# Kernel tuning notes

Hardware: AMD Instinct MI355X
Metric: run time of the kernel (lower is better)

The kernel has to match this reference:

```python
import jax, jax.numpy as jnp
import numpy as np

B = 128          # number of trees
DEPTH = 8        # complete binary tree depth -> 2^8-1 nodes per tree
NPT = 2 ** DEPTH - 1          # 255 nodes per tree
N = B * NPT                   # 32640 total nodes
E_T = NPT - 1                 # 254 edges per tree
F_IN = 64
H = 256


def _build_trees():
    """Complete binary trees; children of local node i are 2i+1, 2i+2."""
    idx = np.arange(NPT)
    depth = np.floor(np.log2(idx + 1)).astype(np.int64)
    order = (DEPTH - 1) - depth                 # leaves=0, root=DEPTH-1
    internal = idx[: NPT // 2]                  # nodes that have children
    parents = np.repeat(internal, 2)
    children = np.empty_like(parents)
    children[0::2] = 2 * internal + 1
    children[1::2] = 2 * internal + 2
    adj_local = np.stack([parents, children], axis=1)        # [E_T, 2]
    offs = (np.arange(B) * NPT)[:, None, None]
    adjacency = (adj_local[None, :, :] + offs).reshape(-1, 2)  # [B*E_T, 2]
    node_order = np.tile(order, B)                             # [N]
    edge_order = np.tile(order[parents], B)                    # [B*E_T]
    return node_order, adjacency, edge_order


def setup_inputs() -> dict:
    key = jax.random.key(0)
    ks = jax.random.split(key, 8)
    node_order, adjacency_list, edge_order = _build_trees()
    s = lambda k, shape, fan: jax.random.normal(k, shape, jnp.float32) * (fan ** -0.5)
    return {
        "features": jax.random.normal(ks[0], (N, F_IN), jnp.float32),
        "node_order": jnp.asarray(node_order, jnp.int32),
        "adjacency_list": jnp.asarray(adjacency_list, jnp.int32),
        "edge_order": jnp.asarray(edge_order, jnp.int32),
        "W_iou_w": s(ks[1], (3 * H, F_IN), F_IN),
        "W_iou_b": jnp.zeros((3 * H,), jnp.float32),
        "U_iou_w": s(ks[2], (3 * H, H), H),
        "W_f_w": s(ks[3], (H, F_IN), F_IN),
        "W_f_b": jnp.zeros((H,), jnp.float32),
        "U_f_w": s(ks[4], (H, H), H),
        "lin0_w": s(ks[5], (H, H), H),
        "lin0_b": jnp.zeros((H,), jnp.float32),
        "lin1_w": s(ks[6], (1, H), H),
        "lin1_b": jnp.zeros((1,), jnp.float32),
    }


def reference(features, node_order, adjacency_list, edge_order,
              W_iou_w, W_iou_b, U_iou_w, W_f_w, W_f_b, U_f_w,
              lin0_w, lin0_b, lin1_w, lin1_b):
    n = features.shape[0]
    parent = adjacency_list[:, 0]
    child = adjacency_list[:, 1]
    # input->gate projections, computed once for all nodes
    wx_iou = features @ W_iou_w.T + W_iou_b      # [N, 3H]
    wx_f = features @ W_f_w.T + W_f_b            # [N, H]
    h = jnp.zeros((n, H), features.dtype)
    c = jnp.zeros((n, H), features.dtype)
    # sequential bottom-up sweep over topological levels (static DEPTH levels)
    for t in range(DEPTH):
        nmask = (node_order == t)[:, None]
        emask = (edge_order == t).astype(features.dtype)[:, None]
        child_h = h[child]                       # [E, H] gather
        h_sum = jax.ops.segment_sum(child_h * emask, parent, num_segments=n)
        iou = wx_iou + h_sum @ U_iou_w.T         # [N, 3H]; h_sum==0 at level 0
        i, o, u = jnp.split(iou, 3, axis=1)
        i = jax.nn.sigmoid(i); o = jax.nn.sigmoid(o); u = jnp.tanh(u)
        f = jax.nn.sigmoid(wx_f[parent] + child_h @ U_f_w.T)  # [E, H]
        c_sum = jax.ops.segment_sum(f * c[child] * emask, parent, num_segments=n)
        new_c = i * u + c_sum
        new_h = o * jnp.tanh(new_c)
        h = jnp.where(nmask, new_h, h)
        c = jnp.where(nmask, new_c, c)
    # unbatch + mean-pool per tree (use_root=False); equal-size trees -> reshape
    x = h.reshape(B, NPT, H).mean(axis=1)        # [B, H]
    # MLP head: Linear -> ReLU -> (dropout inactive in eval) -> Linear
    x = x @ lin0_w.T + lin0_b
    x = jax.nn.relu(x)
    x = x @ lin1_w.T + lin1_b                    # [B, 1]
    return x.reshape(-1)                         # flattened, aux output is None
```

## Files before the change

kernel.cpp:

```cpp
#include <hip/hip_runtime.h>

#define B_TREES 128
#define NPT 255
#define NTOT (B_TREES * NPT)
#define FIN 64
#define HH 256

typedef short bf16x8 __attribute__((ext_vector_type(8)));
typedef float f32x4  __attribute__((ext_vector_type(4)));
typedef unsigned short u16;

__device__ __forceinline__ float sigf(float x) {
    return __frcp_rn(1.0f + __expf(-x));
}
__device__ __forceinline__ float tanh_fast(float x) {
    return __builtin_fmaf(2.0f, sigf(2.0f * x), -1.0f);
}
__device__ __forceinline__ u16 bf_hi(float v) {
    unsigned u = __float_as_uint(v);
    return (u16)((u + 0x7FFFu + ((u >> 16) & 1u)) >> 16);
}
__device__ __forceinline__ float bf_f(u16 b) { return __uint_as_float(((unsigned)b) << 16); }

__global__ __launch_bounds__(256) void pack_B(
    const float* __restrict__ Uiou, const float* __restrict__ Uf,
    const float* __restrict__ Wiou, const float* __restrict__ Wf,
    u16* __restrict__ Bhi, u16* __restrict__ Blo)
{
    int idx = blockIdx.x * 256 + threadIdx.x;
    int j    = idx & 7;
    int lane = (idx >> 3) & 63;
    int ksl  = (idx >> 9) % 10;
    int ct   = idx / 5120;
    int s = ct % 5, hb = ct / 5;
    int n = lane & 15, q = lane >> 4;
    int jH = hb * 16 + n;
    int k = (s < 4 ? ksl * 32 : 320 + ksl * 32) + q * 8 + j;

    float v = 0.0f;
    if (s == 4) {
        if (k < 576) v = Uf[(size_t)jH * HH + (k - 320)];
    } else {
        if (k < 256) {
            v = (s < 3) ? Uiou[(size_t)(s * 256 + jH) * HH + k]
                        : Uf[(size_t)jH * HH + k];
        } else {
            int kw = k - 256;
            v = (s < 3) ? Wiou[(size_t)(s * 256 + jH) * FIN + kw]
                        : 2.0f * Wf[(size_t)jH * FIN + kw];
        }
    }
    u16 hi = bf_hi(v);
    u16 lo = bf_hi(v - bf_f(hi));
    Bhi[idx] = hi;
    Blo[idx] = lo;
}

template<int NCT, bool LEAF>
__global__ __launch_bounds__(256, 2) void level_mfma(
    const float* __restrict__ feat,
    const u16* __restrict__ Bhi, const u16* __restrict__ Blo,
    const float* __restrict__ biou, const float* __restrict__ bfv,
    float* __restrict__ h, float* __restrict__ c,
    int Lt, int lg)
{
    constexpr int CSPLIT = 20 / NCT;
    constexpr int SUBS = NCT / 5;
    __shared__ char smem[73728];
    short* Ahi = (short*)smem;
    short* Alo = (short*)(smem + 36864);

    const int tid = threadIdx.x;
    const int lane = tid & 63, w = tid >> 6;
    const int cs = blockIdx.x % CSPLIT;
    const int rb = blockIdx.x / CSPLIT;
    const int m0 = rb * 32;
    const int msk = (1 << lg) - 1;
    const int ctbase = cs * 4 * NCT + w * NCT;

    const float4* Hf4 = (const float4*)h;
    const float4* Ff4 = (const float4*)feat;

    if constexpr (!LEAF) {
        for (int rep = 0; rep < 8; ++rep) {
            int flat = rep * 256 + tid;
            int m = flat >> 6, f4 = flat & 63;
            int mg = m0 + m;
            int b = mg >> lg, ii = Lt + (mg & msk);
            int gc = b * NPT + 2 * ii + 1;
            float4 h1 = Hf4[(size_t)gc * 64 + f4];
            float4 h2 = Hf4[(size_t)(gc + 1) * 64 + f4];
            float hsv[4] = {h1.x + h2.x, h1.y + h2.y, h1.z + h2.z, h1.w + h2.w};
            float hdv[4] = {h1.x - h2.x, h1.y - h2.y, h1.z - h2.z, h1.w - h2.w};
            int rt = m >> 4, lm = m & 15;
            int ks = f4 >> 3;
            int lane_ = lm + 16 * ((f4 >> 1) & 3);
            int j0 = (f4 & 1) * 4;
            ushort4 sh, sl, dh, dl;
            u16* shp = (u16*)&sh; u16* slp = (u16*)&sl;
            u16* dhp = (u16*)&dh; u16* dlp = (u16*)&dl;
#pragma unroll
            for (int e = 0; e < 4; ++e) {
                u16 a = bf_hi(hsv[e]); shp[e] = a; slp[e] = bf_hi(hsv[e] - bf_f(a));
                u16 d = bf_hi(hdv[e]); dhp[e] = d; dlp[e] = bf_hi(hdv[e] - bf_f(d));
            }
            int base_s = ((rt * 18 + ks) * 64 + lane_) * 8 + j0;
            int base_d = ((rt * 18 + ks + 10) * 64 + lane_) * 8 + j0;
            *(ushort4*)&Ahi[base_s] = sh;  *(ushort4*)&Alo[base_s] = sl;
            *(ushort4*)&Ahi[base_d] = dh;  *(ushort4*)&Alo[base_d] = dl;
        }
    }
    for (int rep = 0; rep < 2; ++rep) {
        int flat = rep * 256 + tid;
        int m = flat >> 4, f4 = flat & 15;
        int mg = m0 + m;
        int b = mg >> lg, ii = Lt + (mg & msk);
        int g = b * NPT + ii;
        float4 x4 = Ff4[(size_t)g * 16 + f4];
        float xv[4] = {x4.x, x4.y, x4.z, x4.w};
        int rt = m >> 4, lm = m & 15;
        int ks = 8 + (f4 >> 3);
        int lane_ = lm + 16 * ((f4 >> 1) & 3);
        int j0 = (f4 & 1) * 4;
        ushort4 xh, xl;
        u16* xhp = (u16*)&xh; u16* xlp = (u16*)&xl;
#pragma unroll
        for (int e = 0; e < 4; ++e) {
            u16 a = bf_hi(xv[e]); xhp[e] = a; xlp[e] = bf_hi(xv[e] - bf_f(a));
        }
        int base = ((rt * 18 + ks) * 64 + lane_) * 8 + j0;
        *(ushort4*)&Ahi[base] = xh;  *(ushort4*)&Alo[base] = xl;
    }
    __syncthreads();

    f32x4 acc[2][NCT];
#pragma unroll
    for (int rt = 0; rt < 2; ++rt)
#pragma unroll
        for (int i = 0; i < NCT; ++i) acc[rt][i] = (f32x4){0.f, 0.f, 0.f, 0.f};

    const int G0 = LEAF ? 8 : 0;
    for (int G = G0; G < 10; ++G) {
        bf16x8 ah[2], al[2];
#pragma unroll
        for (int rt = 0; rt < 2; ++rt) {
            ah[rt] = *(const bf16x8*)&Ahi[((rt * 18 + G) * 64 + lane) * 8];
            al[rt] = *(const bf16x8*)&Alo[((rt * 18 + G) * 64 + lane) * 8];
        }
#pragma unroll
        for (int ctl = 0; ctl < NCT; ++ctl) {
            if (ctl % 5 == 4) continue;
            size_t slot = (size_t)((ctbase + ctl) * 10 + G) * 512 + lane * 8;
            bf16x8 bh = *(const bf16x8*)(Bhi + slot);
            bf16x8 bl = *(const bf16x8*)(Blo + slot);
#pragma unroll
            for (int rt = 0; rt < 2; ++rt) {
                acc[rt][ctl] = __builtin_amdgcn_mfma_f32_16x16x32_bf16(ah[rt], bh, acc[rt][ctl], 0, 0, 0);
                acc[rt][ctl] = __builtin_amdgcn_mfma_f32_16x16x32_bf16(ah[rt], bl, acc[rt][ctl], 0, 0, 0);
                acc[rt][ctl] = __builtin_amdgcn_mfma_f32_16x16x32_bf16(al[rt], bh, acc[rt][ctl], 0, 0, 0);
            }
        }
    }
    if constexpr (!LEAF) {
        for (int G = 10; G < 18; ++G) {
            bf16x8 ah[2], al[2];
#pragma unroll
            for (int rt = 0; rt < 2; ++rt) {
                ah[rt] = *(const bf16x8*)&Ahi[((rt * 18 + G) * 64 + lane) * 8];
                al[rt] = *(const bf16x8*)&Alo[((rt * 18 + G) * 64 + lane) * 8];
            }
#pragma unroll
            for (int ctl = 4; ctl < NCT; ctl += 5) {
                size_t slot = (size_t)((ctbase + ctl) * 10 + (G - 10)) * 512 + lane * 8;
                bf16x8 bh = *(const bf16x8*)(Bhi + slot);
                bf16x8 bl = *(const bf16x8*)(Blo + slot);
#pragma unroll
                for (int rt = 0; rt < 2; ++rt) {
                    acc[rt][ctl] = __builtin_amdgcn_mfma_f32_16x16x32_bf16(ah[rt], bh, acc[rt][ctl], 0, 0, 0);
                    acc[rt][ctl] = __builtin_amdgcn_mfma_f32_16x16x32_bf16(ah[rt], bl, acc[rt][ctl], 0, 0, 0);
                    acc[rt][ctl] = __builtin_amdgcn_mfma_f32_16x16x32_bf16(al[rt], bh, acc[rt][ctl], 0, 0, 0);
                }
            }
        }
    }
    __syncthreads();

    float* sc = (float*)smem + w * 2592;
    const int n = lane & 15, q = lane >> 4;
#pragma unroll
    for (int sub = 0; sub < SUBS; ++sub) {
#pragma unroll
        for (int rt = 0; rt < 2; ++rt)
#pragma unroll
            for (int s = 0; s < 5; ++s) {
                f32x4 v = acc[rt][sub * 5 + s];
#pragma unroll
                for (int r = 0; r < 4; ++r)
                    sc[(rt * 16 + q * 4 + r) * 81 + s * 16 + n] = v[r];
            }
        int hb_abs = ctbase / 5 + sub;
        int jHb = hb_abs * 16;
        for (int it = 0; it < 8; ++it) {
            int idx = it * 64 + lane;
            int m = idx >> 4, jl = idx & 15;
            int jH = jHb + jl;
            float Ci  = sc[m * 81 + jl];
            float Co  = sc[m * 81 + 16 + jl];
            float Cu  = sc[m * 81 + 32 + jl];
            float Cfs = sc[m * 81 + 48 + jl];
            float Cfd = sc[m * 81 + 64 + jl];
            int mg = m0 + m;
            int b = mg >> lg, ii = Lt + (mg & msk);
            size_t g = (size_t)b * NPT + ii;
            float iv = sigf(Ci + biou[jH]);
            float ov = sigf(Co + biou[256 + jH]);
            float uv = tanh_fast(Cu + biou[512 + jH]);
            float cv;
            if constexpr (LEAF) {
                cv = iv * uv;
            } else {
                size_t gc = g + ii + 1;
                float bF = bfv[jH];
                float f1 = sigf(0.5f * (Cfs + Cfd) + bF);
                float f2 = sigf(0.5f * (Cfs - Cfd) + bF);
                cv = iv * uv + f1 * c[gc * HH + jH] + f2 * c[(gc + 1) * HH + jH];
            }
            float hv = ov * tanh_fast(cv);
            c[g * HH + jH] = cv;
            h[g * HH + jH] = hv;
        }
    }
}

__global__ __launch_bounds__(1024) void head_wide(
    const float* __restrict__ h,
    const float* __restrict__ l0w, const float* __restrict__ l0b,
    const float* __restrict__ l1w, const float* __restrict__ l1b,
    float* __restrict__ out)
{
    __shared__ float ms[4][HH];
    __shared__ float part[4][HH];
    __shared__ float red[4];
    int b = blockIdx.x, tid = threadIdx.x;
    int j = tid & 255, g = tid >> 8;
    const float* hb = h + (size_t)b * NPT * HH;

    float a = 0.f;
    for (int i = g; i < NPT; i += 4) a += hb[(size_t)i * HH + j];
    ms[g][j] = a;
    __syncthreads();
    if (g == 0) ms[0][j] = (ms[0][j] + ms[1][j] + ms[2][j] + ms[3][j]) * (1.0f / (float)NPT);
    __syncthreads();

    const float4* L0 = (const float4*)(l0w + (size_t)j * HH);
    float y = 0.f;
    for (int k4 = 16 * g; k4 < 16 * (g + 1); ++k4) {
        float4 wv = L0[k4];
        float4 m4 = ((const float4*)ms[0])[k4];
        y += wv.x * m4.x + wv.y * m4.y + wv.z * m4.z + wv.w * m4.w;
    }
    part[g][j] = y;
    __syncthreads();

    if (g == 0) {
        float yy = part[0][j] + part[1][j] + part[2][j] + part[3][j] + l0b[j];
        yy = fmaxf(yy, 0.f);
        float v = yy * l1w[j];
        for (int off = 32; off > 0; off >>= 1) v += __shfl_down(v, off, 64);
        if ((j & 63) == 0) red[j >> 6] = v;
    }
    __syncthreads();
    if (tid == 0) out[b] = red[0] + red[1] + red[2] + red[3] + l1b[0];
}

extern "C" void kernel_launch(void* const* d_in, const int* in_sizes, int n_in,
                              void* d_out, int out_size, void* d_ws, size_t ws_size,
                              hipStream_t stream)
{
    const float* feat = (const float*)d_in[0];
    const float* Wiou = (const float*)d_in[4];
    const float* biou = (const float*)d_in[5];
    const float* Uiou = (const float*)d_in[6];
    const float* Wf   = (const float*)d_in[7];
    const float* bfv  = (const float*)d_in[8];
    const float* Uf   = (const float*)d_in[9];
    const float* l0w  = (const float*)d_in[10];
    const float* l0b  = (const float*)d_in[11];
    const float* l1w  = (const float*)d_in[12];
    const float* l1b  = (const float*)d_in[13];

    float* h = (float*)d_ws;
    float* c = h + (size_t)NTOT * HH;
    u16* Bhi = (u16*)(c + (size_t)NTOT * HH);
    u16* Blo = Bhi + 409600;

    pack_B<<<1600, 256, 0, stream>>>(Uiou, Uf, Wiou, Wf, Bhi, Blo);

    level_mfma<10, true><<<1024, 256, 0, stream>>>(feat, Bhi, Blo, biou, bfv, h, c, 127, 7);
    level_mfma<10, false><<<512, 256, 0, stream>>>(feat, Bhi, Blo, biou, bfv, h, c, 63, 6);
    level_mfma<5, false><<<512, 256, 0, stream>>>(feat, Bhi, Blo, biou, bfv, h, c, 31, 5);
    level_mfma<5, false><<<256, 256, 0, stream>>>(feat, Bhi, Blo, biou, bfv, h, c, 15, 4);
    level_mfma<5, false><<<128, 256, 0, stream>>>(feat, Bhi, Blo, biou, bfv, h, c, 7, 3);
    level_mfma<5, false><<<64, 256, 0, stream>>>(feat, Bhi, Blo, biou, bfv, h, c, 3, 2);
    level_mfma<5, false><<<32, 256, 0, stream>>>(feat, Bhi, Blo, biou, bfv, h, c, 1, 1);
    level_mfma<5, false><<<16, 256, 0, stream>>>(feat, Bhi, Blo, biou, bfv, h, c, 0, 0);

    head_wide<<<B_TREES, 1024, 0, stream>>>(h, l0w, l0b, l1w, l1b, (float*)d_out);
}
```

Measured before the change: 280.7 us.

## Software-pipeline B-fragment loads and shrink leaf-level LDS and MFMA work

Replaces the nested G/ctl MFMA loops with one fully unrolled step sequence. Global B fragments are prefetched several steps ahead through a register ring buffer, and A fragments are double-buffered from LDS. For leaf levels the LDS footprint is cut to the feature-only K slices, which allows 3 blocks per CU, and the unused forget-gate columns are skipped in the epilogue. Child c values are also loaded in a batch before the gate math so the global loads overlap. The cost is much higher register pressure from the unrolled ring buffer, which could cause spills or lower occupancy.

```diff
diff --git a/kernel.cpp b/kernel.cpp
--- a/kernel.cpp
+++ b/kernel.cpp
@@ -57,7 +57,28 @@
 }
 
 template<int NCT, bool LEAF>
-__global__ __launch_bounds__(256, 2) void level_mfma(
+__device__ __forceinline__ void kdecode(int s, int& G, int& ctl, int& sgB, int& sgA)
+{
+    constexpr int SUBS = NCT / 5;
+    constexpr int TPG  = LEAF ? SUBS * 3 : SUBS * 4;
+    constexpr int MAINS = (LEAF ? 2 : 10) * TPG;
+    if (s < MAINS) {
+        int g = s / TPG, tl = s % TPG;
+        G = (LEAF ? 8 : 0) + g;
+        ctl = LEAF ? (tl / 3) * 5 + (tl % 3) : (tl / 4) * 5 + (tl % 4);
+        sgB = G;
+        sgA = LEAF ? (G - 8) : G;
+    } else {
+        int s2 = s - MAINS;
+        G = 10 + s2 / SUBS;
+        ctl = (s2 % SUBS) * 5 + 4;
+        sgB = G - 10;
+        sgA = G;
+    }
+}
+
+template<int NCT, bool LEAF>
+__global__ __launch_bounds__(256, LEAF ? 3 : 2) void level_mfma(
     const float* __restrict__ feat,
     const u16* __restrict__ Bhi, const u16* __restrict__ Blo,
     const float* __restrict__ biou, const float* __restrict__ bfv,
@@ -66,9 +87,10 @@
 {
     constexpr int CSPLIT = 20 / NCT;
     constexpr int SUBS = NCT / 5;
-    __shared__ char smem[73728];
+    constexpr int KSTR = LEAF ? 2 : 18;
+    __shared__ char smem[LEAF ? 41472 : 73728];
     short* Ahi = (short*)smem;
-    short* Alo = (short*)(smem + 36864);
+    short* Alo = (short*)(smem + (LEAF ? 4096 : 36864));
 
     const int tid = threadIdx.x;
     const int lane = tid & 63, w = tid >> 6;
@@ -119,7 +141,7 @@
         float4 x4 = Ff4[(size_t)g * 16 + f4];
         float xv[4] = {x4.x, x4.y, x4.z, x4.w};
         int rt = m >> 4, lm = m & 15;
-        int ks = 8 + (f4 >> 3);
+        int ks = (LEAF ? 0 : 8) + (f4 >> 3);
         int lane_ = lm + 16 * ((f4 >> 1) & 3);
         int j0 = (f4 & 1) * 4;
         ushort4 xh, xl;
@@ -128,59 +150,74 @@
         for (int e = 0; e < 4; ++e) {
             u16 a = bf_hi(xv[e]); xhp[e] = a; xlp[e] = bf_hi(xv[e] - bf_f(a));
         }
-        int base = ((rt * 18 + ks) * 64 + lane_) * 8 + j0;
+        int base = ((rt * KSTR + ks) * 64 + lane_) * 8 + j0;
         *(ushort4*)&Ahi[base] = xh;  *(ushort4*)&Alo[base] = xl;
     }
     __syncthreads();
 
+    constexpr int TPG    = LEAF ? SUBS * 3 : SUBS * 4;
+    constexpr int MAINS  = (LEAF ? 2 : 10) * TPG;
+    constexpr int NSTEPS = LEAF ? MAINS : MAINS + 8 * SUBS;
+    constexpr int NB = 6, PD = 5;
+    constexpr int GLAST = LEAF ? 9 : 17;
+
     f32x4 acc[2][NCT];
 #pragma unroll
     for (int rt = 0; rt < 2; ++rt)
 #pragma unroll
         for (int i = 0; i < NCT; ++i) acc[rt][i] = (f32x4){0.f, 0.f, 0.f, 0.f};
 
-    const int G0 = LEAF ? 8 : 0;
-    for (int G = G0; G < 10; ++G) {
-        bf16x8 ah[2], al[2];
+    const u16* Bw_h = Bhi + (size_t)ctbase * 5120 + (size_t)lane * 8;
+    const u16* Bw_l = Blo + (size_t)ctbase * 5120 + (size_t)lane * 8;
+    const short* Ah0 = Ahi + lane * 8;
+    const short* Al0 = Alo + lane * 8;
+
+    bf16x8 bh[NB], bl[NB];
+    bf16x8 pah[2][2], pal[2][2];
+
+#pragma unroll
+    for (int rt = 0; rt < 2; ++rt) {
+        pah[0][rt] = *(const bf16x8*)&Ah0[(rt * KSTR + 0) * 512];
+        pal[0][rt] = *(const bf16x8*)&Al0[(rt * KSTR + 0) * 512];
+    }
+#pragma unroll
+    for (int p = 0; p < PD; ++p) {
+        if (p < NSTEPS) {
+            int G2, c2, b2, a2;
+            kdecode<NCT, LEAF>(p, G2, c2, b2, a2);
+            int off = (c2 * 10 + b2) * 512;
+            bh[p % NB] = *(const bf16x8*)(Bw_h + off);
+            bl[p % NB] = *(const bf16x8*)(Bw_l + off);
+        }
+    }
+
+#pragma unroll
+    for (int s = 0; s < NSTEPS; ++s) {
+        int G, ctl, sgB, sgA;
+        kdecode<NCT, LEAF>(s, G, ctl, sgB, sgA);
+        bool firstG = (s < MAINS) ? (s % TPG == 0) : (((s - MAINS) % SUBS) == 0);
+        if (firstG && G < GLAST) {
+            int sgAn = LEAF ? (G - 7) : (G + 1);
+            int parn = (G + 1) & 1;
+#pragma unroll
+            for (int rt = 0; rt < 2; ++rt) {
+                pah[parn][rt] = *(const bf16x8*)&Ah0[(rt * KSTR + sgAn) * 512];
+                pal[parn][rt] = *(const bf16x8*)&Al0[(rt * KSTR + sgAn) * 512];
+            }
+        }
+        if (s + PD < NSTEPS) {
+            int G2, c2, b2, a2;
+            kdecode<NCT, LEAF>(s + PD, G2, c2, b2, a2);
+            int off = (c2 * 10 + b2) * 512;
+            bh[(s + PD) % NB] = *(const bf16x8*)(Bw_h + off);
+            bl[(s + PD) % NB] = *(const bf16x8*)(Bw_l + off);
+        }
+        int par = G & 1;
 #pragma unroll
         for (int rt = 0; rt < 2; ++rt) {
-            ah[rt] = *(const bf16x8*)&Ahi[((rt * 18 + G) * 64 + lane) * 8];
-            al[rt] = *(const bf16x8*)&Alo[((rt * 18 + G) * 64 + lane) * 8];
-        }
-#pragma unroll
-        for (int ctl = 0; ctl < NCT; ++ctl) {
-            if (ctl % 5 == 4) continue;
-            size_t slot = (size_t)((ctbase + ctl) * 10 + G) * 512 + lane * 8;
-            bf16x8 bh = *(const bf16x8*)(Bhi + slot);
-            bf16x8 bl = *(const bf16x8*)(Blo + slot);
-#pragma unroll
-            for (int rt = 0; rt < 2; ++rt) {
-                acc[rt][ctl] = __builtin_amdgcn_mfma_f32_16x16x32_bf16(ah[rt], bh, acc[rt][ctl], 0, 0, 0);
-                acc[rt][ctl] = __builtin_amdgcn_mfma_f32_16x16x32_bf16(ah[rt], bl, acc[rt][ctl], 0, 0, 0);
-                acc[rt][ctl] = __builtin_amdgcn_mfma_f32_16x16x32_bf16(al[rt], bh, acc[rt][ctl], 0, 0, 0);
-            }
-        }
-    }
-    if constexpr (!LEAF) {
-        for (int G = 10; G < 18; ++G) {
-            bf16x8 ah[2], al[2];
-#pragma unroll
-            for (int rt = 0; rt < 2; ++rt) {
-                ah[rt] = *(const bf16x8*)&Ahi[((rt * 18 + G) * 64 + lane) * 8];
-                al[rt] = *(const bf16x8*)&Alo[((rt * 18 + G) * 64 + lane) * 8];
-            }
-#pragma unroll
-            for (int ctl = 4; ctl < NCT; ctl += 5) {
-                size_t slot = (size_t)((ctbase + ctl) * 10 + (G - 10)) * 512 + lane * 8;
-                bf16x8 bh = *(const bf16x8*)(Bhi + slot);
-                bf16x8 bl = *(const bf16x8*)(Blo + slot);
-#pragma unroll
-                for (int rt = 0; rt < 2; ++rt) {
-                    acc[rt][ctl] = __builtin_amdgcn_mfma_f32_16x16x32_bf16(ah[rt], bh, acc[rt][ctl], 0, 0, 0);
-                    acc[rt][ctl] = __builtin_amdgcn_mfma_f32_16x16x32_bf16(ah[rt], bl, acc[rt][ctl], 0, 0, 0);
-                    acc[rt][ctl] = __builtin_amdgcn_mfma_f32_16x16x32_bf16(al[rt], bh, acc[rt][ctl], 0, 0, 0);
-                }
-            }
+            acc[rt][ctl] = __builtin_amdgcn_mfma_f32_16x16x32_bf16(pah[par][rt], bh[s % NB], acc[rt][ctl], 0, 0, 0);
+            acc[rt][ctl] = __builtin_amdgcn_mfma_f32_16x16x32_bf16(pah[par][rt], bl[s % NB], acc[rt][ctl], 0, 0, 0);
+            acc[rt][ctl] = __builtin_amdgcn_mfma_f32_16x16x32_bf16(pal[par][rt], bh[s % NB], acc[rt][ctl], 0, 0, 0);
         }
     }
     __syncthreads();
@@ -192,7 +229,7 @@
 #pragma unroll
         for (int rt = 0; rt < 2; ++rt)
 #pragma unroll
-            for (int s = 0; s < 5; ++s) {
+            for (int s = 0; s < (LEAF ? 3 : 5); ++s) {
                 f32x4 v = acc[rt][sub * 5 + s];
 #pragma unroll
                 for (int r = 0; r < 4; ++r)
@@ -200,6 +237,23 @@
             }
         int hb_abs = ctbase / 5 + sub;
         int jHb = hb_abs * 16;
+
+        float c1v[8], c2v[8];
+        if constexpr (!LEAF) {
+#pragma unroll
+            for (int it = 0; it < 8; ++it) {
+                int idx = it * 64 + lane;
+                int m = idx >> 4, jl = idx & 15;
+                int jH = jHb + jl;
+                int mg = m0 + m;
+                int b = mg >> lg, ii = Lt + (mg & msk);
+                size_t g = (size_t)b * NPT + ii;
+                size_t gc = g + ii + 1;
+                c1v[it] = c[gc * HH + jH];
+                c2v[it] = c[(gc + 1) * HH + jH];
+            }
+        }
+#pragma unroll
         for (int it = 0; it < 8; ++it) {
             int idx = it * 64 + lane;
             int m = idx >> 4, jl = idx & 15;
@@ -207,8 +261,6 @@
             float Ci  = sc[m * 81 + jl];
             float Co  = sc[m * 81 + 16 + jl];
             float Cu  = sc[m * 81 + 32 + jl];
-            float Cfs = sc[m * 81 + 48 + jl];
-            float Cfd = sc[m * 81 + 64 + jl];
             int mg = m0 + m;
             int b = mg >> lg, ii = Lt + (mg & msk);
             size_t g = (size_t)b * NPT + ii;
@@ -219,11 +271,12 @@
             if constexpr (LEAF) {
                 cv = iv * uv;
             } else {
-                size_t gc = g + ii + 1;
+                float Cfs = sc[m * 81 + 48 + jl];
+                float Cfd = sc[m * 81 + 64 + jl];
                 float bF = bfv[jH];
                 float f1 = sigf(0.5f * (Cfs + Cfd) + bF);
                 float f2 = sigf(0.5f * (Cfs - Cfd) + bF);
-                cv = iv * uv + f1 * c[gc * HH + jH] + f2 * c[(gc + 1) * HH + jH];
+                cv = iv * uv + f1 * c1v[it] + f2 * c2v[it];
             }
             float hv = ov * tanh_fast(cv);
             c[g * HH + jH] = cv;
```

Measured after the change: 249.1 us (median of 2 runs). 1.13x faster.
